# Kernel optimization log

Measured on AMD Instinct MI355X. Metric: run time of the kernel, lower is better.

Reference implementation:

```python
import jax, jax.numpy as jnp
import numpy as np

G = 128  # patch size g from __init__


def setup_inputs() -> dict:
    key = jax.random.key(0)
    k1, k2 = jax.random.split(key)
    x = jax.random.normal(k1, (32, 3, 1024, 1024), dtype=jnp.float32)
    l = jax.random.randint(k2, (32, 2), 0, 1024, dtype=jnp.int32)
    return {"x": x, "l": l}


def _foveate(x, l, g):
    B, C, H, W = x.shape
    coords = l.astype(jnp.int32) - 1  # coords = l.long() - 1
    # x_range[i] = (coords - g//2 + i) - g  (the code subtracts an extra `size`)
    offs = jnp.arange(g, dtype=jnp.int32) - (g // 2) - g  # [g]
    rows = coords[:, 0:1] + offs[None, :]  # [B,g], indexes dim 2
    cols = coords[:, 1:2] + offs[None, :]  # [B,g], indexes dim 3
    # bounds check: x_range in range(0, W), y_range in range(0, H)
    valid = ((rows >= 0) & (rows < W))[:, :, None] & ((cols >= 0) & (cols < H))[:, None, :]  # [B,g,g]
    rc = jnp.clip(rows, 0, H - 1)
    cc = jnp.clip(cols, 0, W - 1)
    b_idx = jnp.arange(B)[:, None, None]  # [B,1,1]
    # advanced indexing -> [B,g,g,C]
    gathered = x[b_idx, :, rc[:, :, None], cc[:, None, :]]
    gathered = jnp.where(valid[..., None], gathered, jnp.zeros((), x.dtype))
    patch = jnp.transpose(gathered, (0, 3, 1, 2))  # [B,C,g,g]
    # scatter the (masked) patch back onto a zero canvas; invalid entries add 0
    full = jnp.zeros_like(x).at[b_idx, :, rc[:, :, None], cc[:, None, :]].add(gathered)
    return full, patch


def reference(x, l):
    return _foveate(x, l, G)
```

## Files before the change

kernel.cpp:

```cpp
#include <hip/hip_runtime.h>


#define FULL_ELEMS (32L * 3 * 1024 * 1024)
#define PATCH_ELEMS (32L * 3 * 128 * 128)

__global__ __launch_bounds__(256) void full_fill(const float* __restrict__ x,
                                                 const int* __restrict__ l,
                                                 float* __restrict__ full) {
    long tid = (long)blockIdx.x * 256 + threadIdx.x;
    int w4 = (int)(tid & 255);
    int r  = (int)((tid >> 8) & 1023);
    int b  = (int)(tid / (256L * 1024 * 3));
    int l0 = l[2 * b];
    int l1 = l[2 * b + 1];
    int i = r - (l0 - 193);
    float4 out = make_float4(0.f, 0.f, 0.f, 0.f);
    if ((unsigned)i < 128u) {
        int w0 = w4 * 4;
        int jbase = w0 - (l1 - 193);
        if (jbase >= -3 && jbase < 128) {
            const float4 xin = *(const float4*)(x + tid * 4);
            float v[4] = {xin.x, xin.y, xin.z, xin.w};
            float o[4];
#pragma unroll
            for (int k = 0; k < 4; ++k) {
                int j = jbase + k;
                o[k] = ((unsigned)j < 128u) ? v[k] : 0.f;
            }
            out = make_float4(o[0], o[1], o[2], o[3]);
        }
    }
    *(float4*)(full + tid * 4) = out;
}

__global__ __launch_bounds__(256) void patch_fill(const float* __restrict__ x,
                                                  const int* __restrict__ l,
                                                  float* __restrict__ patch) {
    int tid = blockIdx.x * 256 + threadIdx.x;
    int j4 = tid & 31;
    int i  = (tid >> 5) & 127;
    int c  = (tid >> 12) % 3;
    int b  = tid / (32 * 128 * 3);
    int l0 = l[2 * b];
    int l1 = l[2 * b + 1];
    int r = l0 - 193 + i;
    float o[4] = {0.f, 0.f, 0.f, 0.f};
    if ((unsigned)r < 1024u) {
        const float* xrow = x + (((long)(b * 3 + c) * 1024 + r) << 10);
#pragma unroll
        for (int k = 0; k < 4; ++k) {
            int w = l1 - 193 + j4 * 4 + k;
            if ((unsigned)w < 1024u) o[k] = xrow[w];
        }
    }
    *(float4*)(patch + (long)tid * 4) = make_float4(o[0], o[1], o[2], o[3]);
}

extern "C" void kernel_launch(void* const* d_in, const int* in_sizes, int n_in,
                              void* d_out, int out_size, void* d_ws, size_t ws_size,
                              hipStream_t stream) {
    const float* x = (const float*)d_in[0];
    const int*   l = (const int*)d_in[1];
    float* full  = (float*)d_out;
    float* patch = full + FULL_ELEMS;

    full_fill<<<98304, 256, 0, stream>>>(x, l, full);
    patch_fill<<<1536, 256, 0, stream>>>(x, l, patch);
}
```

Before: 77.72 us.

## Fuse full and patch kernels into one launch with one row per wave

```diff
diff --git a/kernel.cpp b/kernel.cpp
--- a/kernel.cpp
+++ b/kernel.cpp
@@ -1,59 +1,75 @@
 #include <hip/hip_runtime.h>
 
 
-#define FULL_ELEMS (32L * 3 * 1024 * 1024)
+#define FULL_ELEMS  (32L * 3 * 1024 * 1024)
 #define PATCH_ELEMS (32L * 3 * 128 * 128)
 
-__global__ __launch_bounds__(256) void full_fill(const float* __restrict__ x,
-                                                 const int* __restrict__ l,
-                                                 float* __restrict__ full) {
-    long tid = (long)blockIdx.x * 256 + threadIdx.x;
-    int w4 = (int)(tid & 255);
-    int r  = (int)((tid >> 8) & 1023);
-    int b  = (int)(tid / (256L * 1024 * 3));
-    int l0 = l[2 * b];
-    int l1 = l[2 * b + 1];
-    int i = r - (l0 - 193);
-    float4 out = make_float4(0.f, 0.f, 0.f, 0.f);
-    if ((unsigned)i < 128u) {
-        int w0 = w4 * 4;
-        int jbase = w0 - (l1 - 193);
-        if (jbase >= -3 && jbase < 128) {
-            const float4 xin = *(const float4*)(x + tid * 4);
-            float v[4] = {xin.x, xin.y, xin.z, xin.w};
-            float o[4];
+#define FULL_BLOCKS 24576
+#define PATCH_BLOCKS 384
+
+__global__ __launch_bounds__(256) void retina_fused(const float* __restrict__ x,
+                                                    const int* __restrict__ l,
+                                                    float* __restrict__ full,
+                                                    float* __restrict__ patch) {
+    int bid = blockIdx.x;
+    if (bid < FULL_BLOCKS) {
+        int wave = threadIdx.x >> 6;
+        int lane = threadIdx.x & 63;
+        int row  = (bid << 2) + wave;
+        int r    = row & 1023;
+        int bc   = row >> 10;
+        int b    = bc / 3;
+        int l0 = l[2 * b];
+        int l1 = l[2 * b + 1];
+        int i  = r - (l0 - 193);
+        const float4* xrow = (const float4*)(x    + ((long)row << 10));
+        float4*       frow = (float4*)      (full + ((long)row << 10));
+        if ((unsigned)i < 128u) {
+            int jbase0 = -(l1 - 193);
 #pragma unroll
             for (int k = 0; k < 4; ++k) {
-                int j = jbase + k;
-                o[k] = ((unsigned)j < 128u) ? v[k] : 0.f;
+                int w4 = lane + (k << 6);
+                int jb = jbase0 + (w4 << 2);
+                float4 o = make_float4(0.f, 0.f, 0.f, 0.f);
+                if (jb >= -3 && jb < 128) {
+                    float4 v = xrow[w4];
+                    o.x = ((unsigned)(jb + 0) < 128u) ? v.x : 0.f;
+                    o.y = ((unsigned)(jb + 1) < 128u) ? v.y : 0.f;
+                    o.z = ((unsigned)(jb + 2) < 128u) ? v.z : 0.f;
+                    o.w = ((unsigned)(jb + 3) < 128u) ? v.w : 0.f;
+                }
+                frow[w4] = o;
             }
-            out = make_float4(o[0], o[1], o[2], o[3]);
+        } else {
+            float4 z = make_float4(0.f, 0.f, 0.f, 0.f);
+#pragma unroll
+            for (int k = 0; k < 4; ++k) frow[lane + (k << 6)] = z;
+        }
+    } else {
+        int pb = bid - FULL_BLOCKS;
+#pragma unroll
+        for (int k = 0; k < 4; ++k) {
+            int p4 = (pb << 10) + (k << 8) + threadIdx.x;
+            int j4 = p4 & 31;
+            int i  = (p4 >> 5) & 127;
+            int bc = p4 >> 12;
+            int b  = bc / 3;
+            int l0 = l[2 * b];
+            int l1 = l[2 * b + 1];
+            int r  = l0 - 193 + i;
+            float o[4] = {0.f, 0.f, 0.f, 0.f};
+            if ((unsigned)r < 1024u) {
+                const float* xrow = x + (((long)bc << 10) + r) * 1024;
+                int wbase = l1 - 193 + (j4 << 2);
+#pragma unroll
+                for (int e = 0; e < 4; ++e) {
+                    int w = wbase + e;
+                    if ((unsigned)w < 1024u) o[e] = xrow[w];
+                }
+            }
+            *(float4*)(patch + ((long)p4 << 2)) = make_float4(o[0], o[1], o[2], o[3]);
         }
     }
-    *(float4*)(full + tid * 4) = out;
-}
-
-__global__ __launch_bounds__(256) void patch_fill(const float* __restrict__ x,
-                                                  const int* __restrict__ l,
-                                                  float* __restrict__ patch) {
-    int tid = blockIdx.x * 256 + threadIdx.x;
-    int j4 = tid & 31;
-    int i  = (tid >> 5) & 127;
-    int c  = (tid >> 12) % 3;
-    int b  = tid / (32 * 128 * 3);
-    int l0 = l[2 * b];
-    int l1 = l[2 * b + 1];
-    int r = l0 - 193 + i;
-    float o[4] = {0.f, 0.f, 0.f, 0.f};
-    if ((unsigned)r < 1024u) {
-        const float* xrow = x + (((long)(b * 3 + c) * 1024 + r) << 10);
-#pragma unroll
-        for (int k = 0; k < 4; ++k) {
-            int w = l1 - 193 + j4 * 4 + k;
-            if ((unsigned)w < 1024u) o[k] = xrow[w];
-        }
-    }
-    *(float4*)(patch + (long)tid * 4) = make_float4(o[0], o[1], o[2], o[3]);
 }
 
 extern "C" void kernel_launch(void* const* d_in, const int* in_sizes, int n_in,
@@ -63,7 +79,5 @@
     const int*   l = (const int*)d_in[1];
     float* full  = (float*)d_out;
     float* patch = full + FULL_ELEMS;
-
-    full_fill<<<98304, 256, 0, stream>>>(x, l, full);
-    patch_fill<<<1536, 256, 0, stream>>>(x, l, patch);
+    retina_fused<<<FULL_BLOCKS + PATCH_BLOCKS, 256, 0, stream>>>(x, l, full, patch);
 }
```

After: 81.54 us. 1.05x slower.
